# Optimization experiments

Measured on AMD Instinct MI355X. Metric: run time of the kernel, lower is better.

Reference implementation:

```python
import jax, jax.numpy as jnp
import numpy as np

H = 256      # term/query/document hidden size (hardcoded .view(-1, 256) in source)
POS_DIM = 4  # nn.Embedding(15, 4)
V = 50000


def gru_cell(x, h, Wih, Whh, bih, bhh):
    """PyTorch-convention GRU cell. x: [B, Din], h: [B, H]."""
    gi = x @ Wih.T + bih
    gh = h @ Whh.T + bhh
    ir, iz, i_n = jnp.split(gi, 3, axis=-1)
    hr, hz, h_n = jnp.split(gh, 3, axis=-1)
    r = jax.nn.sigmoid(ir + hr)
    z = jax.nn.sigmoid(iz + hz)
    n = jnp.tanh(i_n + r * h_n)
    return (1.0 - z) * n + z * h


def _gru_params(key, in_dim, hid):
    k1, k2, k3, k4 = jax.random.split(key, 4)
    s = 1.0 / np.sqrt(hid)
    u = lambda k, shp: jax.random.uniform(k, shp, jnp.float32, -s, s)
    return u(k1, (3 * hid, in_dim)), u(k2, (3 * hid, hid)), u(k3, (3 * hid,)), u(k4, (3 * hid,))


def setup_inputs() -> dict:
    key = jax.random.key(0)
    ks = jax.random.split(key, 16)
    Q, Lq, P, N, Ld = 64, 20, 12, 12, 50
    inp = {}
    inp["query_tokens"] = jax.random.randint(ks[0], (Q, Lq), 0, V, dtype=jnp.int32)
    inp["pos_tokens"] = jax.random.randint(ks[1], (P, Ld), 0, V, dtype=jnp.int32)
    inp["neg_tokens"] = jax.random.randint(ks[2], (N, Ld), 0, V, dtype=jnp.int32)
    # TermEncoder: embedding + GRU cell
    inp["term_emb"] = jax.random.normal(ks[3], (V, H), jnp.float32) * 0.1
    inp["term_Wih"], inp["term_Whh"], inp["term_bih"], inp["term_bhh"] = _gru_params(ks[4], H, H)
    # ContextEncoder: embedding + two GRU cells (content c, attention a)
    inp["doc_emb"] = jax.random.normal(ks[5], (V, H), jnp.float32) * 0.1
    inp["doc_c_Wih"], inp["doc_c_Whh"], inp["doc_c_bih"], inp["doc_c_bhh"] = _gru_params(ks[6], H, H)
    inp["doc_a_Wih"], inp["doc_a_Whh"], inp["doc_a_bih"], inp["doc_a_bhh"] = _gru_params(ks[7], H, H)
    # position embedding (15, 4) + position_dense Linear(H+4 -> H)
    inp["pos_table"] = jax.random.normal(ks[8], (15, POS_DIM), jnp.float32) * 0.1
    sd = 1.0 / np.sqrt(H + POS_DIM)
    inp["posd_W"] = jax.random.uniform(ks[9], (H, H + POS_DIM), jnp.float32, -sd, sd)
    inp["posd_b"] = jax.random.uniform(ks[10], (H,), jnp.float32, -sd, sd)
    # QueryEncoder GRU cell (single step on the memory-augmented query state)
    inp["qry_Wih"], inp["qry_Whh"], inp["qry_bih"], inp["qry_bhh"] = _gru_params(ks[11], H, H)
    return inp


def reference(query_tokens, pos_tokens, neg_tokens,
              term_emb, term_Wih, term_Whh, term_bih, term_bhh,
              doc_emb, doc_c_Wih, doc_c_Whh, doc_c_bih, doc_c_bhh,
              doc_a_Wih, doc_a_Whh, doc_a_bih, doc_a_bhh,
              pos_table, posd_W, posd_b,
              qry_Wih, qry_Whh, qry_bih, qry_bhh):
    f32 = term_emb.dtype

    # --- TermEncoder: run GRU over each query's tokens (batched over Q queries) ---
    q_xs = term_emb[query_tokens]                       # [Q, Lq, H]
    h0q = jnp.zeros((query_tokens.shape[0], H), f32)
    def term_step(h, x):
        return gru_cell(x, h, term_Wih, term_Whh, term_bih, term_bhh), None
    enc_hidden, _ = jax.lax.scan(term_step, h0q, jnp.swapaxes(q_xs, 0, 1))  # [Q, H]

    # --- ContextEncoder: two parallel GRUs over each doc's tokens (batched over docs) ---
    def encode_docs(tokens):
        xs = doc_emb[tokens]                            # [D, Ld, H]
        h0 = jnp.zeros((tokens.shape[0], H), f32)
        def step(carry, x):
            hc, ha = carry
            hc = gru_cell(x, hc, doc_c_Wih, doc_c_Whh, doc_c_bih, doc_c_bhh)
            ha = gru_cell(x, ha, doc_a_Wih, doc_a_Whh, doc_a_bih, doc_a_bhh)
            return (hc, ha), None
        (hc, ha), _ = jax.lax.scan(step, (h0, h0), jnp.swapaxes(xs, 0, 1))
        # position encoding (pos_enc == 1): concat per-doc-index embedding, dense back to H
        pe = pos_table[jnp.arange(tokens.shape[0])]      # [D, 4]
        hc = jnp.concatenate([hc, pe], axis=-1) @ posd_W.T + posd_b
        return hc, ha                                    # [D, H], [D, H]

    pos_c, pos_a = encode_docs(pos_tokens)
    neg_c, neg_a = encode_docs(neg_tokens)

    # --- memory read: softmax(dot(a_vecs, q)) weighted sum of c_vecs, per query ---
    def attend(c, a_vecs, q):
        scores = q @ a_vecs.T                            # [Q, D]
        w = jax.nn.softmax(scores, axis=-1)
        return w @ c                                     # [Q, H]

    q_pos_neg = enc_hidden + attend(pos_c, pos_a, enc_hidden) + attend(neg_c, neg_a, enc_hidden)

    # --- QueryEncoder: one GRU step on the memory-augmented state ---
    h0 = jnp.zeros_like(q_pos_neg)
    q_out = gru_cell(q_pos_neg, h0, qry_Wih, qry_Whh, qry_bih, qry_bhh)  # [Q, H]
    return q_out
```

## Files before the change

### kernel.cpp

```cpp
#include <hip/hip_runtime.h>
#include <hip/hip_fp16.h>
#include <math.h>

#define H 256

typedef _Float16 f16x8 __attribute__((ext_vector_type(8)));
typedef _Float16 f16x4 __attribute__((ext_vector_type(4)));
typedef float    f32x4 __attribute__((ext_vector_type(4)));
typedef _Float16 h2_t  __attribute__((ext_vector_type(2)));
union U16x8 { uint4 u; h2_t h[4]; };

#define WS_WF_T  0u
#define WS_WF_C  98304u
#define WS_WF_A  196608u
#define WS_W16T  294912u
#define WS_W16C  393216u
#define WS_W16A  491520u
#define WS_W16Q  589824u
#define WS_PT    688128u
#define WS_GI_T  754688u
#define WS_GI_C  1737728u
#define WS_GI_A  2659328u
#define WS_ENC   3580928u
#define WS_HC    3597312u
#define WS_HA    3603456u

__device__ __forceinline__ float sigmoidf_(float x){ return 1.f/(1.f+expf(-x)); }

__global__ __launch_bounds__(256) void k_prep2(
    const float* __restrict__ tWhh, const float* __restrict__ cWhh, const float* __restrict__ aWhh,
    const float* __restrict__ tWih, const float* __restrict__ cWih, const float* __restrict__ aWih,
    const float* __restrict__ qWih, const float* __restrict__ pdW,
    _Float16* __restrict__ WFt, _Float16* __restrict__ WFc, _Float16* __restrict__ WFa,
    _Float16* __restrict__ W16t, _Float16* __restrict__ W16c, _Float16* __restrict__ W16a,
    _Float16* __restrict__ W16q, float* __restrict__ PT)
{
    const int b = blockIdx.x, tid = threadIdx.x;
    if (b < 2304) {
        int i = b * 256 + tid;
        int m = i / 196608, r = i % 196608;
        const float* in = (m == 0) ? tWhh : (m == 1) ? cWhh : aWhh;
        _Float16*   out = (m == 0) ? WFt  : (m == 1) ? WFc  : WFa;
        int f = r >> 9, lane = (r >> 3) & 63, e = r & 7;
        int row = (f >> 3) * 16 + (lane & 15);
        int k   = (f & 7) * 32 + ((lane >> 4) & 3) * 8 + e;
        out[r] = (_Float16)in[row * 256 + k];
        return;
    }
    if (b < 5376) {
        int i = (b - 2304) * 256 + tid;
        int m = i / 196608, r = i % 196608;
        const float* in = (m == 0) ? tWih : (m == 1) ? cWih : (m == 2) ? aWih : qWih;
        _Float16*   out = (m == 0) ? W16t : (m == 1) ? W16c : (m == 2) ? W16a : W16q;
        out[r] = (_Float16)in[r];
        return;
    }
    {
        int i = (b - 5376) * 256 + tid;
        int k = i >> 8, j = i & 255;
        PT[k * 256 + j] = pdW[j * 260 + k];
    }
}

__global__ __launch_bounds__(256) void k_gi2(
    const int* __restrict__ qtok, const int* __restrict__ ptok, const int* __restrict__ ntok,
    const float* __restrict__ temb, const float* __restrict__ demb,
    const _Float16* __restrict__ W16t, const _Float16* __restrict__ W16c, const _Float16* __restrict__ W16a,
    const float* __restrict__ tbih, const float* __restrict__ cbih, const float* __restrict__ abih,
    float* __restrict__ git, float* __restrict__ gic, float* __restrict__ gia)
{
    __shared__ __align__(16) _Float16 At[64 * 264];
    __shared__ int tok[64];

    const int bid = blockIdx.x, tid = threadIdx.x;
    const float *emb, *bih; const _Float16* W16; float* out; int nrows, seg, mt, nt;
    if (bid < 240)      { seg = 0; int b = bid;       mt = b / 12; nt = b % 12; emb = temb; W16 = W16t; bih = tbih; out = git; nrows = 1280; }
    else if (bid < 468) { seg = 1; int b = bid - 240; mt = b / 12; nt = b % 12; emb = demb; W16 = W16c; bih = cbih; out = gic; nrows = 1200; }
    else                { seg = 2; int b = bid - 468; mt = b / 12; nt = b % 12; emb = demb; W16 = W16a; bih = abih; out = gia; nrows = 1200; }
    const int rowbase = mt * 64, jb = nt * 64;

    if (tid < 64) {
        int rg = rowbase + tid;
        int token = 0;
        if (rg < nrows) {
            if (seg == 0) { int t = mt, q = tid; token = qtok[q * 20 + t]; }
            else          { int t = rg / 24, d = rg % 24; token = (d < 12) ? ptok[d * 50 + t] : ntok[(d - 12) * 50 + t]; }
        }
        tok[tid] = token;
    }
    __syncthreads();

#pragma unroll
    for (int i = 0; i < 16; i++) {
        int idx = i * 256 + tid;
        int r = idx >> 6, c4 = idx & 63;
        float4 v = *(const float4*)(emb + (size_t)tok[r] * H + c4 * 4);
        f16x4 hv = { (_Float16)v.x, (_Float16)v.y, (_Float16)v.z, (_Float16)v.w };
        *(f16x4*)(At + r * 264 + c4 * 4) = hv;
    }
    __syncthreads();

    const int wave = tid >> 6, lane = tid & 63;
    const int rt = wave;
    const int kg = (lane >> 4) & 3;

    f16x8 af[8];
    const _Float16* abase = At + (rt * 16 + (lane & 15)) * 264 + kg * 8;
#pragma unroll
    for (int kt = 0; kt < 8; kt++) af[kt] = *(const f16x8*)(abase + kt * 32);

#pragma unroll
    for (int ct = 0; ct < 4; ct++) {
        const int col = jb + ct * 16 + (lane & 15);
        const _Float16* wrow = W16 + (size_t)col * H + kg * 8;
        f32x4 acc = {0.f, 0.f, 0.f, 0.f};
#pragma unroll
        for (int kt = 0; kt < 8; kt++) {
            f16x8 bf = *(const f16x8*)(wrow + kt * 32);
            acc = __builtin_amdgcn_mfma_f32_16x16x32_f16(af[kt], bf, acc, 0, 0, 0);
        }
        float bias = bih[col];
#pragma unroll
        for (int e = 0; e < 4; e++) {
            int row_g = rowbase + rt * 16 + kg * 4 + e;
            if (row_g < nrows)
                out[(size_t)row_g * 768 + col] = acc[e] + bias;
        }
    }
}

__global__ __launch_bounds__(768) void k_recur5(
    const _Float16* __restrict__ WFt, const _Float16* __restrict__ WFc, const _Float16* __restrict__ WFa,
    const float* __restrict__ tbhh, const float* __restrict__ cbhh, const float* __restrict__ abhh,
    const float* __restrict__ gi_t, const float* __restrict__ gi_c, const float* __restrict__ gi_a,
    float* __restrict__ enc, float* __restrict__ hc, float* __restrict__ ha)
{
    __shared__ __align__(16) _Float16 hhl[H];
    __shared__ __align__(16) float    ghl[768];

    const int b = blockIdx.x, tid = threadIdx.x;
    const _Float16* WF; const float *bhh, *gi; float* outp; int T, nch, chain;
    if (b < 64)      { WF = WFt; bhh = tbhh; gi = gi_t; T = 20; nch = 64; chain = b;      outp = enc; }
    else if (b < 88) { WF = WFc; bhh = cbhh; gi = gi_c; T = 50; nch = 24; chain = b - 64; outp = hc; }
    else             { WF = WFa; bhh = abhh; gi = gi_a; T = 50; nch = 24; chain = b - 88; outp = ha; }

    const int wave = tid >> 6, lane = tid & 63;
    const int grp = (lane >> 4) & 3;
    const bool extr = (lane & 15) == 0;

    const f16x8* __restrict__ WFp = (const f16x8*)WF;
    f16x8 wf[32];
#pragma unroll
    for (int i = 0; i < 32; i++) wf[i] = WFp[(size_t)(wave * 32 + i) * 64 + lane];
    asm volatile("" ::: "memory");

    float h = 0.f, br = 0.f, bz = 0.f, bn = 0.f;
    if (tid < H) {
        br = bhh[tid]; bz = bhh[tid + 256]; bn = bhh[tid + 512];
        hhl[tid] = (_Float16)0.f;
    }
    __syncthreads();

    for (int t = 0; t < T; t++) {
        f32x4 acc0 = {0.f,0.f,0.f,0.f}, acc1 = {0.f,0.f,0.f,0.f};
        f32x4 acc2 = {0.f,0.f,0.f,0.f}, acc3 = {0.f,0.f,0.f,0.f};
#pragma unroll
        for (int kt = 0; kt < 8; kt++) {
            f16x8 bv = {0,0,0,0,0,0,0,0};
            if (extr) bv = *(const f16x8*)(hhl + kt * 32 + grp * 8);
            acc0 = __builtin_amdgcn_mfma_f32_16x16x32_f16(wf[0 * 8 + kt], bv, acc0, 0, 0, 0);
            acc1 = __builtin_amdgcn_mfma_f32_16x16x32_f16(wf[1 * 8 + kt], bv, acc1, 0, 0, 0);
            acc2 = __builtin_amdgcn_mfma_f32_16x16x32_f16(wf[2 * 8 + kt], bv, acc2, 0, 0, 0);
            acc3 = __builtin_amdgcn_mfma_f32_16x16x32_f16(wf[3 * 8 + kt], bv, acc3, 0, 0, 0);
        }
        if (extr) {
            *(f32x4*)(ghl + wave * 64 +  0 + grp * 4) = acc0;
            *(f32x4*)(ghl + wave * 64 + 16 + grp * 4) = acc1;
            *(f32x4*)(ghl + wave * 64 + 32 + grp * 4) = acc2;
            *(f32x4*)(ghl + wave * 64 + 48 + grp * 4) = acc3;
        }
        __syncthreads();
        if (tid < H) {
            const float* __restrict__ grow = gi + (size_t)(t * nch + chain) * 768;
            float r = sigmoidf_(grow[tid]       + br + ghl[tid]);
            float z = sigmoidf_(grow[tid + 256] + bz + ghl[tid + 256]);
            float n = tanhf(grow[tid + 512] + r * (bn + ghl[tid + 512]));
            h = (1.f - z) * n + z * h;
            hhl[tid] = (_Float16)h;
        }
        __syncthreads();
    }
    if (tid < H) outp[(size_t)chain * H + tid] = h;
}

__global__ __launch_bounds__(256) void k_final2(
    const float* __restrict__ enc, const float* __restrict__ ha, const float* __restrict__ hc,
    const float* __restrict__ ptab, const float* __restrict__ PT, const float* __restrict__ pdb,
    const _Float16* __restrict__ qW16, const float* __restrict__ qbih, const float* __restrict__ qbhh,
    float* __restrict__ out)
{
    __shared__ __align__(16) float ql[H];
    __shared__ __align__(16) float csl[H];
    __shared__ float csp[4];
    __shared__ float wts[24];
    __shared__ __align__(16) _Float16 q2h[H];

    const int q = blockIdx.x, j = threadIdx.x;
    ql[j] = enc[q * H + j];
    __syncthreads();

    if (j < 192) {
        int dd = j >> 3, l8 = j & 7;
        float s = 0.f;
        for (int k = l8 * 32; k < l8 * 32 + 32; k++) s += ha[dd * H + k] * ql[k];
        s += __shfl_xor(s, 1); s += __shfl_xor(s, 2); s += __shfl_xor(s, 4);
        if (l8 == 0) wts[dd] = s;
    }
    __syncthreads();
    if (j < 2) {
        int base = j * 12;
        float m = wts[base];
        for (int d = 1; d < 12; d++) m = fmaxf(m, wts[base + d]);
        float sum = 0.f;
        for (int d = 0; d < 12; d++) { float e = expf(wts[base + d] - m); wts[base + d] = e; sum += e; }
        float inv = 1.f / sum;
        for (int d = 0; d < 12; d++) wts[base + d] *= inv;
    }
    __syncthreads();

    {
        float cs = 0.f;
#pragma unroll 4
        for (int d = 0; d < 24; d++) cs += wts[d] * hc[d * H + j];
        csl[j] = cs;
    }
    if (j < 4) {
        float cp = 0.f;
        for (int d = 0; d < 24; d++) cp += wts[d] * ptab[(d % 12) * 4 + j];
        csp[j] = cp;
    }
    __syncthreads();

    float att = 2.f * pdb[j];
#pragma unroll 4
    for (int k = 0; k < 256; k++) att += csl[k] * PT[(size_t)k * 256 + j];
#pragma unroll
    for (int k = 0; k < 4; k++)   att += csp[k] * PT[(size_t)(256 + k) * 256 + j];

    float q2 = ql[j] + att;
    q2h[j] = (_Float16)q2;
    __syncthreads();

    const uint4* q4 = (const uint4*)q2h;
    const uint4* w0 = (const uint4*)(qW16 + (size_t)(j      ) * H);
    const uint4* w1 = (const uint4*)(qW16 + (size_t)(j + 256) * H);
    const uint4* w2 = (const uint4*)(qW16 + (size_t)(j + 512) * H);
    float ar = 0.f, az = 0.f, an = 0.f;
#pragma unroll 8
    for (int k8 = 0; k8 < 32; k8++) {
        U16x8 hv; hv.u = q4[k8];
        U16x8 a; a.u = w0[k8];
        U16x8 bb; bb.u = w1[k8];
        U16x8 c; c.u = w2[k8];
#pragma unroll
        for (int p = 0; p < 4; p++) {
            ar = __builtin_amdgcn_fdot2(a.h[p],  hv.h[p], ar, false);
            az = __builtin_amdgcn_fdot2(bb.h[p], hv.h[p], az, false);
            an = __builtin_amdgcn_fdot2(c.h[p],  hv.h[p], an, false);
        }
    }
    float r = sigmoidf_(ar + qbih[j]       + qbhh[j]);
    float z = sigmoidf_(az + qbih[j + 256] + qbhh[j + 256]);
    float n = tanhf(an + qbih[j + 512] + r * qbhh[j + 512]);
    out[q * H + j] = (1.f - z) * n;
}

extern "C" void kernel_launch(void* const* d_in, const int* in_sizes, int n_in,
                              void* d_out, int out_size, void* d_ws, size_t ws_size,
                              hipStream_t stream)
{
    const int*   qtok = (const int*)d_in[0];
    const int*   ptok = (const int*)d_in[1];
    const int*   ntok = (const int*)d_in[2];
    const float* temb = (const float*)d_in[3];
    const float* tWih = (const float*)d_in[4];
    const float* tWhh = (const float*)d_in[5];
    const float* tbih = (const float*)d_in[6];
    const float* tbhh = (const float*)d_in[7];
    const float* demb = (const float*)d_in[8];
    const float* cWih = (const float*)d_in[9];
    const float* cWhh = (const float*)d_in[10];
    const float* cbih = (const float*)d_in[11];
    const float* cbhh = (const float*)d_in[12];
    const float* aWih = (const float*)d_in[13];
    const float* aWhh = (const float*)d_in[14];
    const float* abih = (const float*)d_in[15];
    const float* abhh = (const float*)d_in[16];
    const float* ptab = (const float*)d_in[17];
    const float* pdW  = (const float*)d_in[18];
    const float* pdb  = (const float*)d_in[19];
    const float* qWih = (const float*)d_in[20];
    const float* qbih = (const float*)d_in[22];
    const float* qbhh = (const float*)d_in[23];

    float* ws = (float*)d_ws;
    _Float16* WFt  = (_Float16*)(ws + WS_WF_T);
    _Float16* WFc  = (_Float16*)(ws + WS_WF_C);
    _Float16* WFa  = (_Float16*)(ws + WS_WF_A);
    _Float16* W16t = (_Float16*)(ws + WS_W16T);
    _Float16* W16c = (_Float16*)(ws + WS_W16C);
    _Float16* W16a = (_Float16*)(ws + WS_W16A);
    _Float16* W16q = (_Float16*)(ws + WS_W16Q);
    float* PT  = ws + WS_PT;
    float* GIt = ws + WS_GI_T;
    float* GIc = ws + WS_GI_C;
    float* GIa = ws + WS_GI_A;
    float* ENC = ws + WS_ENC;
    float* HC  = ws + WS_HC;
    float* HA  = ws + WS_HA;

    k_prep2<<<5636, 256, 0, stream>>>(tWhh, cWhh, aWhh, tWih, cWih, aWih, qWih, pdW,
                                      WFt, WFc, WFa, W16t, W16c, W16a, W16q, PT);

    k_gi2<<<696, 256, 0, stream>>>(qtok, ptok, ntok, temb, demb,
                                   W16t, W16c, W16a, tbih, cbih, abih,
                                   GIt, GIc, GIa);

    k_recur5<<<112, 768, 0, stream>>>(WFt, WFc, WFa, tbhh, cbhh, abhh,
                                      GIt, GIc, GIa, ENC, HC, HA);

    k_final2<<<64, 256, 0, stream>>>(ENC, HA, HC, ptab, PT, pdb,
                                     W16q, qbih, qbhh, (float*)d_out);
}
```

Baseline: 293.5 us.

## Batch 16 GRU chains per block in recurrence MFMA and store input gates in fp16

The recurrence kernel now packs up to 16 independent chains into the 16 MFMA columns, where before each block wasted 15 of the 16 columns on one chain. It runs 8 blocks instead of 112, so each block loads the Whh fragments once for many chains, and the elementwise gate update is spread over all 768 threads. The precomputed input-gate activations are written and read as fp16 instead of fp32, which halves that traffic. In exchange, each serial step now does about 12-16 times more elementwise gate work per block, only 8 CUs are used, and fp16 rounding of the gate inputs slightly lowers precision.

```diff
diff --git a/kernel.cpp b/kernel.cpp
--- a/kernel.cpp
+++ b/kernel.cpp
@@ -67,13 +67,13 @@
     const float* __restrict__ temb, const float* __restrict__ demb,
     const _Float16* __restrict__ W16t, const _Float16* __restrict__ W16c, const _Float16* __restrict__ W16a,
     const float* __restrict__ tbih, const float* __restrict__ cbih, const float* __restrict__ abih,
-    float* __restrict__ git, float* __restrict__ gic, float* __restrict__ gia)
+    _Float16* __restrict__ git, _Float16* __restrict__ gic, _Float16* __restrict__ gia)
 {
     __shared__ __align__(16) _Float16 At[64 * 264];
     __shared__ int tok[64];
 
     const int bid = blockIdx.x, tid = threadIdx.x;
-    const float *emb, *bih; const _Float16* W16; float* out; int nrows, seg, mt, nt;
+    const float *emb, *bih; const _Float16* W16; _Float16* out; int nrows, seg, mt, nt;
     if (bid < 240)      { seg = 0; int b = bid;       mt = b / 12; nt = b % 12; emb = temb; W16 = W16t; bih = tbih; out = git; nrows = 1280; }
     else if (bid < 468) { seg = 1; int b = bid - 240; mt = b / 12; nt = b % 12; emb = demb; W16 = W16c; bih = cbih; out = gic; nrows = 1200; }
     else                { seg = 2; int b = bid - 468; mt = b / 12; nt = b % 12; emb = demb; W16 = W16a; bih = abih; out = gia; nrows = 1200; }
@@ -124,73 +124,88 @@
         for (int e = 0; e < 4; e++) {
             int row_g = rowbase + rt * 16 + kg * 4 + e;
             if (row_g < nrows)
-                out[(size_t)row_g * 768 + col] = acc[e] + bias;
-        }
-    }
-}
-
-__global__ __launch_bounds__(768) void k_recur5(
+                out[(size_t)row_g * 768 + col] = (_Float16)(acc[e] + bias);
+        }
+    }
+}
+
+__global__ __launch_bounds__(768, 3) void k_recur6(
     const _Float16* __restrict__ WFt, const _Float16* __restrict__ WFc, const _Float16* __restrict__ WFa,
     const float* __restrict__ tbhh, const float* __restrict__ cbhh, const float* __restrict__ abhh,
-    const float* __restrict__ gi_t, const float* __restrict__ gi_c, const float* __restrict__ gi_a,
+    const _Float16* __restrict__ gi_t, const _Float16* __restrict__ gi_c, const _Float16* __restrict__ gi_a,
     float* __restrict__ enc, float* __restrict__ hc, float* __restrict__ ha)
 {
-    __shared__ __align__(16) _Float16 hhl[H];
-    __shared__ __align__(16) float    ghl[768];
+    __shared__ __align__(16) _Float16 hh[16][264];
+    __shared__ __align__(16) float    hf[16][260];
+    __shared__ __align__(16) float    gh[16][780];
+    __shared__ float bg[768];
 
     const int b = blockIdx.x, tid = threadIdx.x;
-    const _Float16* WF; const float *bhh, *gi; float* outp; int T, nch, chain;
-    if (b < 64)      { WF = WFt; bhh = tbhh; gi = gi_t; T = 20; nch = 64; chain = b;      outp = enc; }
-    else if (b < 88) { WF = WFc; bhh = cbhh; gi = gi_c; T = 50; nch = 24; chain = b - 64; outp = hc; }
-    else             { WF = WFa; bhh = abhh; gi = gi_a; T = 50; nch = 24; chain = b - 88; outp = ha; }
+    const _Float16* WF; const float* bhh; const _Float16* gi; float* outp;
+    int T, nch_g, ch0, ncl;
+    if (b < 4)      { WF = WFt; bhh = tbhh; gi = gi_t; T = 20; nch_g = 64; ch0 = b * 16;       ncl = 16; outp = enc; }
+    else if (b < 6) { WF = WFc; bhh = cbhh; gi = gi_c; T = 50; nch_g = 24; ch0 = (b - 4) * 12; ncl = 12; outp = hc; }
+    else            { WF = WFa; bhh = abhh; gi = gi_a; T = 50; nch_g = 24; ch0 = (b - 6) * 12; ncl = 12; outp = ha; }
 
     const int wave = tid >> 6, lane = tid & 63;
-    const int grp = (lane >> 4) & 3;
-    const bool extr = (lane & 15) == 0;
+    const int chn = lane & 15;
+    const int kq  = lane >> 4;
 
     const f16x8* __restrict__ WFp = (const f16x8*)WF;
     f16x8 wf[32];
 #pragma unroll
     for (int i = 0; i < 32; i++) wf[i] = WFp[(size_t)(wave * 32 + i) * 64 + lane];
-    asm volatile("" ::: "memory");
-
-    float h = 0.f, br = 0.f, bz = 0.f, bn = 0.f;
-    if (tid < H) {
-        br = bhh[tid]; bz = bhh[tid + 256]; bn = bhh[tid + 512];
-        hhl[tid] = (_Float16)0.f;
-    }
+
+    bg[tid] = bhh[tid];
+    for (int i = tid; i < 16 * 264; i += 768) ((_Float16*)hh)[i] = (_Float16)0.f;
+    for (int i = tid; i < 16 * 260; i += 768) ((float*)hf)[i] = 0.f;
     __syncthreads();
 
     for (int t = 0; t < T; t++) {
+#pragma unroll
+        for (int i = 0; i < 32; i++) asm volatile("" : "+v"(wf[i]));
+
         f32x4 acc0 = {0.f,0.f,0.f,0.f}, acc1 = {0.f,0.f,0.f,0.f};
         f32x4 acc2 = {0.f,0.f,0.f,0.f}, acc3 = {0.f,0.f,0.f,0.f};
 #pragma unroll
         for (int kt = 0; kt < 8; kt++) {
-            f16x8 bv = {0,0,0,0,0,0,0,0};
-            if (extr) bv = *(const f16x8*)(hhl + kt * 32 + grp * 8);
-            acc0 = __builtin_amdgcn_mfma_f32_16x16x32_f16(wf[0 * 8 + kt], bv, acc0, 0, 0, 0);
-            acc1 = __builtin_amdgcn_mfma_f32_16x16x32_f16(wf[1 * 8 + kt], bv, acc1, 0, 0, 0);
-            acc2 = __builtin_amdgcn_mfma_f32_16x16x32_f16(wf[2 * 8 + kt], bv, acc2, 0, 0, 0);
-            acc3 = __builtin_amdgcn_mfma_f32_16x16x32_f16(wf[3 * 8 + kt], bv, acc3, 0, 0, 0);
-        }
-        if (extr) {
-            *(f32x4*)(ghl + wave * 64 +  0 + grp * 4) = acc0;
-            *(f32x4*)(ghl + wave * 64 + 16 + grp * 4) = acc1;
-            *(f32x4*)(ghl + wave * 64 + 32 + grp * 4) = acc2;
-            *(f32x4*)(ghl + wave * 64 + 48 + grp * 4) = acc3;
+            f16x8 bv = *(const f16x8*)&hh[chn][kt * 32 + kq * 8];
+            acc0 = __builtin_amdgcn_mfma_f32_16x16x32_f16(wf[kt],      bv, acc0, 0, 0, 0);
+            acc1 = __builtin_amdgcn_mfma_f32_16x16x32_f16(wf[8 + kt],  bv, acc1, 0, 0, 0);
+            acc2 = __builtin_amdgcn_mfma_f32_16x16x32_f16(wf[16 + kt], bv, acc2, 0, 0, 0);
+            acc3 = __builtin_amdgcn_mfma_f32_16x16x32_f16(wf[24 + kt], bv, acc3, 0, 0, 0);
+        }
+        {
+            const int r0 = wave * 64 + kq * 4;
+            *(f32x4*)&gh[chn][r0     ] = acc0;
+            *(f32x4*)&gh[chn][r0 + 16] = acc1;
+            *(f32x4*)&gh[chn][r0 + 32] = acc2;
+            *(f32x4*)&gh[chn][r0 + 48] = acc3;
         }
         __syncthreads();
-        if (tid < H) {
-            const float* __restrict__ grow = gi + (size_t)(t * nch + chain) * 768;
-            float r = sigmoidf_(grow[tid]       + br + ghl[tid]);
-            float z = sigmoidf_(grow[tid + 256] + bz + ghl[tid + 256]);
-            float n = tanhf(grow[tid + 512] + r * (bn + ghl[tid + 512]));
-            h = (1.f - z) * n + z * h;
-            hhl[tid] = (_Float16)h;
+
+        for (int p = 0; p < 6; p++) {
+            int idx = p * 768 + tid;
+            int c = idx >> 8, j = idx & 255;
+            if (c < ncl) {
+                const _Float16* __restrict__ grow = gi + (size_t)(t * nch_g + ch0 + c) * 768;
+                float gr = (float)grow[j], gz = (float)grow[j + 256], gn = (float)grow[j + 512];
+                float r = sigmoidf_(gr + bg[j]       + gh[c][j]);
+                float z = sigmoidf_(gz + bg[j + 256] + gh[c][j + 256]);
+                float n = tanhf(gn + r * (bg[j + 512] + gh[c][j + 512]));
+                float hn = (1.f - z) * n + z * hf[c][j];
+                hf[c][j] = hn;
+                hh[c][j] = (_Float16)hn;
+            }
         }
         __syncthreads();
     }
-    if (tid < H) outp[(size_t)chain * H + tid] = h;
+
+    for (int p = 0; p < 6; p++) {
+        int idx = p * 768 + tid;
+        int c = idx >> 8, j = idx & 255;
+        if (c < ncl) outp[(size_t)(ch0 + c) * H + j] = hf[c][j];
+    }
 }
 
 __global__ __launch_bounds__(256) void k_final2(
@@ -312,9 +327,9 @@
     _Float16* W16a = (_Float16*)(ws + WS_W16A);
     _Float16* W16q = (_Float16*)(ws + WS_W16Q);
     float* PT  = ws + WS_PT;
-    float* GIt = ws + WS_GI_T;
-    float* GIc = ws + WS_GI_C;
-    float* GIa = ws + WS_GI_A;
+    _Float16* GIt = (_Float16*)(ws + WS_GI_T);
+    _Float16* GIc = (_Float16*)(ws + WS_GI_C);
+    _Float16* GIa = (_Float16*)(ws + WS_GI_A);
     float* ENC = ws + WS_ENC;
     float* HC  = ws + WS_HC;
     float* HA  = ws + WS_HA;
@@ -326,8 +341,8 @@
                                    W16t, W16c, W16a, tbih, cbih, abih,
                                    GIt, GIc, GIa);
 
-    k_recur5<<<112, 768, 0, stream>>>(WFt, WFc, WFa, tbhh, cbhh, abhh,
-                                      GIt, GIc, GIa, ENC, HC, HA);
+    k_recur6<<<8, 768, 0, stream>>>(WFt, WFc, WFa, tbhh, cbhh, abhh,
+                                    GIt, GIc, GIa, ENC, HC, HA);
 
     k_final2<<<64, 256, 0, stream>>>(ENC, HA, HC, ptab, PT, pdb,
                                      W16q, qbih, qbhh, (float*)d_out);
```

Measured after the change: 407.9 us. 39.0% more time.
